# Optimization experiments

Hardware: AMD Instinct MI355X
Metric: run time of the kernel (lower is better)

## Reference

```python
import jax, jax.numpy as jnp
import numpy as np

B, N, F_IN, H, C, K = 32, 1024, 128, 64, 32, 2
L_HOP, NUM_ITER, TEMP = 2, 5, 0.5


def setup_inputs() -> dict:
    key = jax.random.key(0)
    ks = jax.random.split(key, 8)
    x = jax.random.normal(ks[0], (B, N, F_IN), jnp.float32)
    adj = jax.random.randint(ks[1], (B, N, N), 0, 2, jnp.int32)  # dense 0/1 adjacency per graph
    W_gcn = jax.random.normal(ks[2], (F_IN, H), jnp.float32) / np.sqrt(F_IN)
    b_gcn = jnp.zeros((H,), jnp.float32)
    W_unary = jax.random.normal(ks[3], (H, C), jnp.float32) / np.sqrt(H)
    b_unary = jnp.zeros((C,), jnp.float32)
    means = jax.random.normal(ks[4], (K, H), jnp.float32)
    scales = jnp.ones((K, H), jnp.float32) * 8.0  # widened so exp(-dist) stays in fp32 range
    kw = jnp.ones((K,), jnp.float32)
    mu = jax.random.normal(ks[5], (C, C), jnp.float32)
    return dict(x=x, adj=adj, W_gcn=W_gcn, b_gcn=b_gcn, W_unary=W_unary,
                b_unary=b_unary, means=means, scales=scales, kw=kw, mu=mu)


def _forward(x, adj_f, W_gcn, b_gcn, W_unary, b_unary, means, scales, kw, mu):
    n = x.shape[1]
    # --- GCN encode: D^{-1/2}(A+I)D^{-1/2} X W + b, relu ---
    a_hat = adj_f + jnp.eye(n, dtype=adj_f.dtype)
    dinv = jax.lax.rsqrt(a_hat.sum(-1))                       # [B,N], deg >= 1 via self-loop
    norm = dinv[:, :, None] * a_hat * dinv[:, None, :]        # [B,N,N]
    h = jax.nn.relu(jnp.einsum('bij,bjf,fh->bih', norm, x, W_gcn) + b_gcn)  # [B,N,H]
    # --- l-hop reachability mask ---
    adj_l = adj_f
    for _ in range(L_HOP - 1):
        adj_l = adj_l @ adj_f
    adj_l = (adj_l > 0).astype(h.dtype)                       # [B,N,N]
    # --- unary potentials ---
    unary = h @ W_unary + b_unary                             # [B,N,C]
    # --- Gaussian kernel: w_k * exp(dist_i[k] + dist_j[k]) == (e*w) @ e.T ---
    diff = (h[:, :, None, :] - means) / scales                # [B,N,K,H]
    e = jnp.exp(-jnp.sum(diff * diff, -1))                    # [B,N,K]
    pairwise = jnp.einsum('bik,k,bjk->bij', e, kw, e) * adj_l  # [B,N,N]
    # --- mean-field CRF iterations ---
    Q = jax.nn.softmax(unary, -1)
    for _ in range(NUM_ITER):
        msg = jnp.einsum('bij,bjc->bic', pairwise, Q @ mu)
        Q = jax.nn.softmax((unary + msg) / TEMP, -1)
    # --- soft-cluster pooling ---
    x_pooled = jnp.einsum('bnc,bnh->bch', Q, h)               # [B,C,H]
    adj_pooled = jnp.einsum('bnc,bnm,bmd->bcd', Q, adj_f, Q)  # [B,C,C]
    return x_pooled, adj_pooled


def reference(x, adj, W_gcn, b_gcn, W_unary, b_unary, means, scales, kw, mu):
    return _forward(x, adj.astype(x.dtype), W_gcn, b_gcn, W_unary, b_unary,
                    means, scales, kw, mu)
```

## Files before the change

### kernel.cpp

```cpp
#include <hip/hip_runtime.h>
#include <stdint.h>

#define NB  32
#define NN  1024
#define FIN 128
#define HH  64
#define CC  32
#define ZCAP 16
#define NITER 5

using short8  = __attribute__((ext_vector_type(8))) short;
using floatx4 = __attribute__((ext_vector_type(4))) float;

__device__ inline float b2f(unsigned short u) {
  union { uint32_t i; float f; } v; v.i = ((uint32_t)u) << 16; return v.f;
}
__device__ inline unsigned short f2b(float f) {
  union { uint32_t i; float f; } v; v.f = f;
  uint32_t r = v.i + 0x7FFFu + ((v.i >> 16) & 1u);
  return (unsigned short)(r >> 16);
}
__device__ inline floatx4 zf4() { floatx4 v = {0.f, 0.f, 0.f, 0.f}; return v; }

__global__ __launch_bounds__(256) void k_wcvt(const float* __restrict__ Wg,
    const float* __restrict__ Wu, unsigned short* __restrict__ Wgt,
    unsigned short* __restrict__ Wut, float* __restrict__ out, int out_n) {
  const int t = threadIdx.x;
  for (int idx = t; idx < HH * FIN; idx += 256) {
    int hh = idx >> 7, f = idx & 127;
    Wgt[idx] = f2b(Wg[f * HH + hh]);
  }
  for (int idx = t; idx < CC * HH; idx += 256) {
    int c = idx >> 6, f = idx & 63;
    Wut[idx] = f2b(Wu[f * CC + c]);
  }
  for (int idx = t; idx < out_n; idx += 256) out[idx] = 0.f;
}

__global__ __launch_bounds__(256) void k_bits(const int* __restrict__ adj,
    uint32_t* __restrict__ rowbits, float* __restrict__ dinv,
    int* __restrict__ zcnt) {
  __shared__ uint32_t rw[4][32];
  const int t = threadIdx.x, g = t >> 6, lane = t & 63;
  if (lane < 32) rw[g][lane] = 0u;
  __syncthreads();
  const size_t row = (size_t)blockIdx.x * 4 + g;
  int s = 0;
  #pragma unroll
  for (int rep = 0; rep < 4; rep++) {
    int4 a = ((const int4*)(adj + row * NN))[rep * 64 + lane];
    int b0 = (a.x != 0), b1 = (a.y != 0), b2 = (a.z != 0), b3 = (a.w != 0);
    uint32_t nib = ((uint32_t)(b0 | (b1 << 1) | (b2 << 2) | (b3 << 3))) << ((lane & 7) * 4);
    atomicOr(&rw[g][rep * 8 + (lane >> 3)], nib);
    s += b0 + b1 + b2 + b3;
  }
  #pragma unroll
  for (int m = 1; m < 64; m <<= 1) s += __shfl_xor(s, m, 64);
  __syncthreads();
  if (lane < 32) rowbits[row * 32 + lane] = rw[g][lane];
  if (lane == 0) { dinv[row] = rsqrtf((float)s + 1.0f); zcnt[row] = 0; }
}

__global__ __launch_bounds__(256) void k_cbits(const uint32_t* __restrict__ rowbits,
    uint32_t* __restrict__ colbits) {
  __shared__ uint32_t rbL[512 * 32];
  const int bid = blockIdx.x;
  const int b = bid >> 3, half = (bid >> 2) & 1, jt = bid & 3;
  const int t = threadIdx.x;
  const uint32_t* src = rowbits + ((size_t)b * NN + half * 512) * 32;
  for (int idx = t; idx < 512 * 32; idx += 256) rbL[idx] = src[idx];
  __syncthreads();
  const int j = jt * 256 + t, jw = j >> 5, jb = j & 31;
  uint32_t out[16];
  for (int w = 0; w < 16; w++) {
    uint32_t acc = 0;
    #pragma unroll
    for (int r = 0; r < 32; r++)
      acc |= ((rbL[(w * 32 + r) * 32 + jw] >> jb) & 1u) << r;
    out[w] = acc;
  }
  uint4* dst = (uint4*)(colbits + ((size_t)b * NN + j) * 32 + half * 16);
  #pragma unroll
  for (int x = 0; x < 4; x++) {
    uint4 v; v.x = out[4*x]; v.y = out[4*x+1]; v.z = out[4*x+2]; v.w = out[4*x+3];
    dst[x] = v;
  }
}

__global__ __launch_bounds__(256) void k_xw(const float* __restrict__ x,
    const unsigned short* __restrict__ Wgt, const float* __restrict__ dinv,
    unsigned short* __restrict__ xs, unsigned short* __restrict__ xst) {
  const int bid = blockIdx.x;
  const int b = bid >> 4;
  const int m0 = (bid & 15) * 64;
  const int t = threadIdx.x, wv = t >> 6, lane = t & 63, l15 = lane & 15, q = lane >> 4;
  const int mb = m0 + wv * 16;
  floatx4 acc[4];
  #pragma unroll
  for (int u = 0; u < 4; u++) acc[u] = zf4();
  #pragma unroll
  for (int k0 = 0; k0 < FIN; k0 += 32) {
    const float4* xp = (const float4*)(x + ((size_t)b * NN + mb + l15) * FIN + k0 + q * 8);
    float4 a0 = xp[0], a1 = xp[1];
    short8 af;
    af[0] = (short)f2b(a0.x); af[1] = (short)f2b(a0.y);
    af[2] = (short)f2b(a0.z); af[3] = (short)f2b(a0.w);
    af[4] = (short)f2b(a1.x); af[5] = (short)f2b(a1.y);
    af[6] = (short)f2b(a1.z); af[7] = (short)f2b(a1.w);
    #pragma unroll
    for (int u = 0; u < 4; u++) {
      short8 bf = *(const short8*)(Wgt + (u * 16 + l15) * FIN + k0 + q * 8);
      acc[u] = __builtin_amdgcn_mfma_f32_16x16x32_bf16(af, bf, acc[u], 0, 0, 0);
    }
  }
  #pragma unroll
  for (int r = 0; r < 4; r++) {
    const int i = mb + q * 4 + r;
    const float dv = dinv[b * NN + i];
    #pragma unroll
    for (int u = 0; u < 4; u++) {
      const int c = u * 16 + l15;
      unsigned short bv = f2b(dv * acc[u][r]);
      xs[((size_t)b * NN + i) * HH + c] = bv;
      xst[((size_t)b * HH + c) * NN + i] = bv;
    }
  }
}

__global__ __launch_bounds__(256) void k_gcnun(const uint32_t* __restrict__ rowbits,
    const unsigned short* __restrict__ xst, const unsigned short* __restrict__ xs,
    const float* __restrict__ dinv, const float* __restrict__ bg,
    const float* __restrict__ means, const float* __restrict__ scales,
    const unsigned short* __restrict__ Wut, const float* __restrict__ bu,
    float* __restrict__ h, float* __restrict__ e2, float* __restrict__ unary,
    float* __restrict__ Q0) {
  __shared__ unsigned short hsh[4][16][72];
  const int bid = blockIdx.x;
  const int b = bid >> 4;
  const int m0 = (bid & 15) * 64;
  const int t = threadIdx.x, wv = t >> 6, lane = t & 63, l15 = lane & 15, q = lane >> 4;
  const int mb = m0 + wv * 16;
  floatx4 acc[4];
  #pragma unroll
  for (int u = 0; u < 4; u++) acc[u] = zf4();
  const uint32_t* rbrow = rowbits + ((size_t)b * NN + mb + l15) * 32;
  for (int k0 = 0; k0 < NN; k0 += 32) {
    uint32_t sh = rbrow[k0 >> 5] >> (q * 8);
    short8 af;
    #pragma unroll
    for (int jj = 0; jj < 8; jj++)
      af[jj] = (short)(((sh >> jj) & 1u) ? 0x3F80 : 0);
    #pragma unroll
    for (int u = 0; u < 4; u++) {
      short8 bf = *(const short8*)(xst + ((size_t)b * HH + u * 16 + l15) * NN + k0 + q * 8);
      acc[u] = __builtin_amdgcn_mfma_f32_16x16x32_bf16(af, bf, acc[u], 0, 0, 0);
    }
  }
  float bgc[4], mn0[4], mn1[4], is0[4], is1[4];
  #pragma unroll
  for (int u = 0; u < 4; u++) {
    const int c = u * 16 + l15;
    bgc[u] = bg[c];
    mn0[u] = means[c];        is0[u] = 1.0f / scales[c];
    mn1[u] = means[HH + c];   is1[u] = 1.0f / scales[HH + c];
  }
  #pragma unroll
  for (int r = 0; r < 4; r++) {
    const int i = mb + q * 4 + r;
    const float dv = dinv[b * NN + i];
    float dd0 = 0.f, dd1 = 0.f;
    #pragma unroll
    for (int u = 0; u < 4; u++) {
      const int c = u * 16 + l15;
      float xsv = b2f(xs[((size_t)b * NN + i) * HH + c]);
      float v = dv * (acc[u][r] + xsv) + bgc[u];
      v = v > 0.f ? v : 0.f;
      h[((size_t)b * NN + i) * HH + c] = v;
      unsigned short hb = f2b(v);
      hsh[wv][q * 4 + r][c] = hb;
      float vb = b2f(hb);
      float t0 = (vb - mn0[u]) * is0[u]; dd0 += t0 * t0;
      float t1 = (vb - mn1[u]) * is1[u]; dd1 += t1 * t1;
    }
    #pragma unroll
    for (int m = 1; m < 16; m <<= 1) {
      dd0 += __shfl_xor(dd0, m, 64);
      dd1 += __shfl_xor(dd1, m, 64);
    }
    if (l15 == 0) {
      e2[((size_t)b * NN + i) * 2 + 0] = __expf(-dd0);
      e2[((size_t)b * NN + i) * 2 + 1] = __expf(-dd1);
    }
  }
  floatx4 uacc[2];
  uacc[0] = zf4(); uacc[1] = zf4();
  #pragma unroll
  for (int k0 = 0; k0 < HH; k0 += 32) {
    short8 af = *(const short8*)&hsh[wv][l15][k0 + q * 8];
    #pragma unroll
    for (int u = 0; u < 2; u++) {
      short8 bf = *(const short8*)(Wut + (u * 16 + l15) * HH + k0 + q * 8);
      uacc[u] = __builtin_amdgcn_mfma_f32_16x16x32_bf16(af, bf, uacc[u], 0, 0, 0);
    }
  }
  const float bu0 = bu[l15], bu1 = bu[16 + l15];
  #pragma unroll
  for (int r = 0; r < 4; r++) {
    const int i = mb + q * 4 + r;
    float a0 = uacc[0][r] + bu0;
    float a1 = uacc[1][r] + bu1;
    unary[((size_t)b * NN + i) * CC + l15] = a0;
    unary[((size_t)b * NN + i) * CC + 16 + l15] = a1;
    float mx = fmaxf(a0, a1);
    #pragma unroll
    for (int m = 1; m < 16; m <<= 1) mx = fmaxf(mx, __shfl_xor(mx, m, 64));
    float x0 = __expf(a0 - mx), x1 = __expf(a1 - mx);
    float s = x0 + x1;
    #pragma unroll
    for (int m = 1; m < 16; m <<= 1) s += __shfl_xor(s, m, 64);
    float inv = 1.f / s;
    Q0[((size_t)b * NN + i) * CC + l15] = x0 * inv;
    Q0[((size_t)b * NN + i) * CC + 16 + l15] = x1 * inv;
  }
}

__global__ __launch_bounds__(256) void k_zscan(const uint32_t* __restrict__ rowbits,
    const uint32_t* __restrict__ colbits, int* __restrict__ zcnt,
    int* __restrict__ zidx) {
  __shared__ uint32_t rwL[128 * 32];
  const int bid = blockIdx.x;
  const int b = bid >> 3, it = bid & 7;
  const int i0 = it * 128;
  const int t = threadIdx.x;
  #pragma unroll
  for (int x = 0; x < 16; x++)
    rwL[x * 256 + t] = rowbits[((size_t)b * NN + i0) * 32 + x * 256 + t];
  __syncthreads();
  for (int jc = 0; jc < 4; jc++) {
    const int j = jc * 256 + t;
    uint32_t cb[32];
    const uint4* cbp = (const uint4*)(colbits + ((size_t)b * NN + j) * 32);
    #pragma unroll
    for (int x = 0; x < 8; x++) {
      uint4 v = cbp[x];
      cb[4*x] = v.x; cb[4*x+1] = v.y; cb[4*x+2] = v.z; cb[4*x+3] = v.w;
    }
    for (int i = 0; i < 128; i++) {
      uint32_t m = 0;
      for (int w = 0; w < 32; w++) {
        m |= rwL[i * 32 + w] & cb[w];
        if (__all(m != 0)) break;
      }
      if (m == 0) {
        int old = atomicAdd(&zcnt[b * NN + i0 + i], 1);
        if (old < ZCAP) zidx[(size_t)(b * NN + i0 + i) * ZCAP + old] = j;
      }
    }
  }
}

__global__ __launch_bounds__(256) void k_titer(const float* __restrict__ e2,
    const float* __restrict__ Q, float* __restrict__ Tpart) {
  __shared__ float part[4][64];
  const int bid = blockIdx.x;
  const int b = bid >> 2, qd = bid & 3;
  const int t = threadIdx.x, kd = t & 63, d = t & 31, k = (t >> 5) & 1, sub = t >> 6;
  const float* e2b = e2 + (size_t)b * NN * 2;
  const float* Qb  = Q + (size_t)b * NN * CC;
  const int j0 = qd * 256 + sub * 64;
  float s = 0.f;
  #pragma unroll 8
  for (int jj = 0; jj < 64; jj++) {
    const int j = j0 + jj;
    s += e2b[j * 2 + k] * Qb[j * CC + d];
  }
  part[sub][kd] = s;
  __syncthreads();
  if (t < 64)
    Tpart[(size_t)bid * 64 + t] = part[0][t] + part[1][t] + part[2][t] + part[3][t];
}

__global__ __launch_bounds__(256) void k_supd(const float* __restrict__ unary,
    const float* __restrict__ e2, const float* __restrict__ Tpart,
    const float* __restrict__ mu, const float* __restrict__ kwp,
    const int* __restrict__ zcnt, const int* __restrict__ zidx,
    const uint32_t* __restrict__ rowbits, const uint32_t* __restrict__ colbits,
    const float* __restrict__ Qin, float* __restrict__ Qout,
    unsigned short* __restrict__ qtb, int last) {
  __shared__ float muL[CC * CC];
  __shared__ float Ts[64];
  __shared__ float S[64];
  const int bid = blockIdx.x;
  const int b = bid >> 2, seg = bid & 3;
  const int t = threadIdx.x;
  for (int i = t; i < CC * CC; i += 256) muL[i] = mu[i];
  if (t < 64)
    Ts[t] = Tpart[(size_t)(b * 4 + 0) * 64 + t] + Tpart[(size_t)(b * 4 + 1) * 64 + t]
          + Tpart[(size_t)(b * 4 + 2) * 64 + t] + Tpart[(size_t)(b * 4 + 3) * 64 + t];
  __syncthreads();
  if (t < 64) {
    const int k = t >> 5, c = t & 31;
    float s = 0.f;
    #pragma unroll 8
    for (int d = 0; d < CC; d++) s += Ts[k * 32 + d] * muL[d * 32 + c];
    S[t] = ((k == 0) ? kwp[0] : kwp[1]) * s;
  }
  __syncthreads();
  const int n = seg * 256 + t;
  const int gid = b * NN + n;
  const float e0 = e2[(size_t)gid * 2 + 0];
  const float e1 = e2[(size_t)gid * 2 + 1];
  float lg[CC];
  {
    const float4* urow = (const float4*)(unary + (size_t)gid * CC);
    const float4* S0 = (const float4*)S;
    const float4* S1 = (const float4*)(S + 32);
    #pragma unroll
    for (int c4 = 0; c4 < 8; c4++) {
      float4 uv = urow[c4], s0 = S0[c4], s1 = S1[c4];
      lg[c4*4]   = uv.x + e0 * s0.x + e1 * s1.x;
      lg[c4*4+1] = uv.y + e0 * s0.y + e1 * s1.y;
      lg[c4*4+2] = uv.z + e0 * s0.z + e1 * s1.z;
      lg[c4*4+3] = uv.w + e0 * s0.w + e1 * s1.w;
    }
  }
  const int zc = zcnt[gid];
  if (zc > 0) {
    const float kw0 = kwp[0], kw1 = kwp[1];
    if (zc <= ZCAP) {
      for (int z = 0; z < zc; z++) {
        const int j = zidx[(size_t)gid * ZCAP + z];
        const float w = kw0 * e0 * e2[((size_t)b * NN + j) * 2 + 0]
                      + kw1 * e1 * e2[((size_t)b * NN + j) * 2 + 1];
        const float* qj = Qin + ((size_t)b * NN + j) * CC;
        for (int d = 0; d < CC; d++) {
          const float wq = w * qj[d];
          #pragma unroll 8
          for (int c = 0; c < CC; c++) lg[c] -= wq * muL[d * CC + c];
        }
      }
    } else {
      const uint32_t* rbi = rowbits + (size_t)gid * 32;
      for (int j = 0; j < NN; j++) {
        uint32_t m = 0;
        const uint32_t* cbj = colbits + ((size_t)b * NN + j) * 32;
        for (int w32 = 0; w32 < 32; w32++) m |= rbi[w32] & cbj[w32];
        if (m == 0) {
          const float w = kw0 * e0 * e2[((size_t)b * NN + j) * 2 + 0]
                        + kw1 * e1 * e2[((size_t)b * NN + j) * 2 + 1];
          const float* qj = Qin + ((size_t)b * NN + j) * CC;
          for (int d = 0; d < CC; d++) {
            const float wq = w * qj[d];
            #pragma unroll 8
            for (int c = 0; c < CC; c++) lg[c] -= wq * muL[d * CC + c];
          }
        }
      }
    }
  }
  float mx = lg[0];
  #pragma unroll
  for (int c = 1; c < CC; c++) mx = fmaxf(mx, lg[c]);
  float s = 0.f;
  #pragma unroll
  for (int c = 0; c < CC; c++) { lg[c] = __expf((lg[c] - mx) * 2.0f); s += lg[c]; }
  float inv = 1.f / s;
  float4* qo = (float4*)(Qout + (size_t)gid * CC);
  #pragma unroll
  for (int c4 = 0; c4 < 8; c4++) {
    float4 v;
    v.x = lg[c4*4] * inv; v.y = lg[c4*4+1] * inv;
    v.z = lg[c4*4+2] * inv; v.w = lg[c4*4+3] * inv;
    qo[c4] = v;
  }
  if (last) {
    #pragma unroll
    for (int c = 0; c < CC; c++)
      qtb[((size_t)b * CC + c) * NN + n] = f2b(lg[c] * inv);
  }
}

__global__ __launch_bounds__(256) void k_adjq(const uint32_t* __restrict__ rowbits,
    const unsigned short* __restrict__ qtb, float* __restrict__ adjQ) {
  const int bid = blockIdx.x;
  const int b = bid >> 4;
  const int m0 = (bid & 15) * 64;
  const int t = threadIdx.x, wv = t >> 6, lane = t & 63, l15 = lane & 15, q = lane >> 4;
  const int mb = m0 + wv * 16;
  floatx4 acc[2];
  acc[0] = zf4(); acc[1] = zf4();
  const uint32_t* rbrow = rowbits + ((size_t)b * NN + mb + l15) * 32;
  for (int k0 = 0; k0 < NN; k0 += 32) {
    uint32_t sh = rbrow[k0 >> 5] >> (q * 8);
    short8 af;
    #pragma unroll
    for (int jj = 0; jj < 8; jj++)
      af[jj] = (short)(((sh >> jj) & 1u) ? 0x3F80 : 0);
    #pragma unroll
    for (int u = 0; u < 2; u++) {
      short8 bf = *(const short8*)(qtb + ((size_t)b * CC + u * 16 + l15) * NN + k0 + q * 8);
      acc[u] = __builtin_amdgcn_mfma_f32_16x16x32_bf16(af, bf, acc[u], 0, 0, 0);
    }
  }
  #pragma unroll
  for (int r = 0; r < 4; r++) {
    const int i = mb + q * 4 + r;
    #pragma unroll
    for (int u = 0; u < 2; u++)
      adjQ[((size_t)b * NN + i) * CC + u * 16 + l15] = acc[u][r];
  }
}

__global__ __launch_bounds__(256) void k_pool(const float* __restrict__ Q,
    const float* __restrict__ h, const float* __restrict__ adjQ,
    float* __restrict__ out) {
  const int bid = blockIdx.x;
  const int t = threadIdx.x;
  if (bid < NB * 4) {
    const int b = bid >> 2, jc = bid & 3;
    const int hh = t & 63, cg = t >> 6;
    float acc[8] = {0, 0, 0, 0, 0, 0, 0, 0};
    for (int jj = 0; jj < 256; jj++) {
      const int j = jc * 256 + jj;
      float hv = h[((size_t)b * NN + j) * HH + hh];
      const float* qr = Q + ((size_t)b * NN + j) * CC + cg * 8;
      #pragma unroll
      for (int k = 0; k < 8; k++) acc[k] += qr[k] * hv;
    }
    #pragma unroll
    for (int k = 0; k < 8; k++)
      atomicAdd(&out[((size_t)b * CC + cg * 8 + k) * HH + hh], acc[k]);
  } else {
    const int bid2 = bid - NB * 4;
    const int b = bid2 >> 2, jc = bid2 & 3;
    const int d = t & 31, cg = t >> 5;
    float acc[4] = {0, 0, 0, 0};
    for (int jj = 0; jj < 256; jj++) {
      const int j = jc * 256 + jj;
      float av = adjQ[((size_t)b * NN + j) * CC + d];
      const float* qr = Q + ((size_t)b * NN + j) * CC + cg * 4;
      #pragma unroll
      for (int k = 0; k < 4; k++) acc[k] += qr[k] * av;
    }
    #pragma unroll
    for (int k = 0; k < 4; k++)
      atomicAdd(&out[(size_t)NB * CC * HH + ((size_t)b * CC + cg * 4 + k) * CC + d], acc[k]);
  }
}

extern "C" void kernel_launch(void* const* d_in, const int* in_sizes, int n_in,
                              void* d_out, int out_size, void* d_ws, size_t ws_size,
                              hipStream_t stream) {
  (void)in_sizes; (void)n_in; (void)out_size;
  const float* x      = (const float*)d_in[0];
  const int*   adj    = (const int*)d_in[1];
  const float* Wg     = (const float*)d_in[2];
  const float* bg     = (const float*)d_in[3];
  const float* Wu     = (const float*)d_in[4];
  const float* bu     = (const float*)d_in[5];
  const float* means  = (const float*)d_in[6];
  const float* scales = (const float*)d_in[7];
  const float* kw     = (const float*)d_in[8];
  const float* mu     = (const float*)d_in[9];

  char* ws = (char*)d_ws;
  size_t off = 0;
  auto alloc = [&](size_t bytes) { char* p = ws + off; off += (bytes + 255) & ~(size_t)255; return p; };
  uint32_t*       rbits = (uint32_t*)alloc((size_t)NB * NN * 32 * 4);
  uint32_t*       cbits = (uint32_t*)alloc((size_t)NB * NN * 32 * 4);
  float*          dinv  = (float*)alloc((size_t)NB * NN * 4);
  unsigned short* Wgt   = (unsigned short*)alloc((size_t)HH * FIN * 2);
  unsigned short* Wut   = (unsigned short*)alloc((size_t)CC * HH * 2);
  unsigned short* xs    = (unsigned short*)alloc((size_t)NB * NN * HH * 2);
  unsigned short* xst   = (unsigned short*)alloc((size_t)NB * HH * NN * 2);
  float*          h     = (float*)alloc((size_t)NB * NN * HH * 4);
  float*          e2    = (float*)alloc((size_t)NB * NN * 2 * 4);
  float*          unary = (float*)alloc((size_t)NB * NN * CC * 4);
  int*            zcnt  = (int*)alloc((size_t)NB * NN * 4);
  int*            zidx  = (int*)alloc((size_t)NB * NN * ZCAP * 4);
  float*          Qa    = (float*)alloc((size_t)NB * NN * CC * 4);
  float*          Qb    = (float*)alloc((size_t)NB * NN * CC * 4);
  unsigned short* qtb   = (unsigned short*)alloc((size_t)NB * CC * NN * 2);
  float*          adjQ  = (float*)alloc((size_t)NB * NN * CC * 4);
  float*          Tpart = (float*)alloc((size_t)NB * 4 * 64 * 4);
  if (off > ws_size) return;

  float* out = (float*)d_out;
  const int out_n = NB * CC * (HH + CC);

  k_wcvt <<<1, 256, 0, stream>>>(Wg, Wu, Wgt, Wut, out, out_n);
  k_bits <<<NB * NN / 4, 256, 0, stream>>>(adj, rbits, dinv, zcnt);
  k_cbits<<<NB * 8, 256, 0, stream>>>(rbits, cbits);
  k_xw   <<<NB * 16, 256, 0, stream>>>(x, Wgt, dinv, xs, xst);
  k_gcnun<<<NB * 16, 256, 0, stream>>>(rbits, xst, xs, dinv, bg, means, scales,
                                       Wut, bu, h, e2, unary, Qa);
  k_zscan<<<NB * 8, 256, 0, stream>>>(rbits, cbits, zcnt, zidx);
  float* qin = Qa; float* qout = Qb;
  for (int it = 0; it < NITER; it++) {
    k_titer<<<NB * 4, 256, 0, stream>>>(e2, qin, Tpart);
    k_supd <<<NB * 4, 256, 0, stream>>>(unary, e2, Tpart, mu, kw, zcnt, zidx,
                                        rbits, cbits, qin, qout, qtb,
                                        it == NITER - 1 ? 1 : 0);
    float* tmp = qin; qin = qout; qout = tmp;
  }
  k_adjq <<<NB * 16, 256, 0, stream>>>(rbits, qtb, adjQ);
  k_pool <<<NB * 8, 256, 0, stream>>>(qin, h, adjQ, out);
}
```

Before: 428.9 us.

## Fuse all CRF iterations and pooling into a single per-graph LDS-resident kernel

Replaces the ten per-iteration titer/supd launches with one kernel that keeps each graph's Q (packed bf16) and e2 in shared memory and runs all five mean-field iterations with block-level syncs. The initial softmax moves into this kernel, and Q·h pooling is fused at its end. The adjacency-Q product and the adj pooling are merged into one kernel through shared-memory staging. This removes launch overhead and global Q round trips, but each graph's redundant 4 blocks each recompute all 1024 nodes, and Q is held in bf16 during iterations, lowering precision.

```diff
diff --git a/kernel.cpp b/kernel.cpp
--- a/kernel.cpp
+++ b/kernel.cpp
@@ -14,6 +14,12 @@
 
 __device__ inline float b2f(unsigned short u) {
   union { uint32_t i; float f; } v; v.i = ((uint32_t)u) << 16; return v.f;
+}
+__device__ inline float b2f_lo(uint32_t w) {
+  union { uint32_t i; float f; } v; v.i = w << 16; return v.f;
+}
+__device__ inline float b2f_hi(uint32_t w) {
+  union { uint32_t i; float f; } v; v.i = w & 0xFFFF0000u; return v.f;
 }
 __device__ inline unsigned short f2b(float f) {
   union { uint32_t i; float f; } v; v.f = f;
@@ -132,8 +138,7 @@
     const float* __restrict__ dinv, const float* __restrict__ bg,
     const float* __restrict__ means, const float* __restrict__ scales,
     const unsigned short* __restrict__ Wut, const float* __restrict__ bu,
-    float* __restrict__ h, float* __restrict__ e2, float* __restrict__ unary,
-    float* __restrict__ Q0) {
+    float* __restrict__ h, float* __restrict__ e2, float* __restrict__ unary) {
   __shared__ unsigned short hsh[4][16][72];
   const int bid = blockIdx.x;
   const int b = bid >> 4;
@@ -207,20 +212,8 @@
   #pragma unroll
   for (int r = 0; r < 4; r++) {
     const int i = mb + q * 4 + r;
-    float a0 = uacc[0][r] + bu0;
-    float a1 = uacc[1][r] + bu1;
-    unary[((size_t)b * NN + i) * CC + l15] = a0;
-    unary[((size_t)b * NN + i) * CC + 16 + l15] = a1;
-    float mx = fmaxf(a0, a1);
-    #pragma unroll
-    for (int m = 1; m < 16; m <<= 1) mx = fmaxf(mx, __shfl_xor(mx, m, 64));
-    float x0 = __expf(a0 - mx), x1 = __expf(a1 - mx);
-    float s = x0 + x1;
-    #pragma unroll
-    for (int m = 1; m < 16; m <<= 1) s += __shfl_xor(s, m, 64);
-    float inv = 1.f / s;
-    Q0[((size_t)b * NN + i) * CC + l15] = x0 * inv;
-    Q0[((size_t)b * NN + i) * CC + 16 + l15] = x1 * inv;
+    unary[((size_t)b * NN + i) * CC + l15] = uacc[0][r] + bu0;
+    unary[((size_t)b * NN + i) * CC + 16 + l15] = uacc[1][r] + bu1;
   }
 }
 
@@ -259,129 +252,173 @@
   }
 }
 
-__global__ __launch_bounds__(256) void k_titer(const float* __restrict__ e2,
-    const float* __restrict__ Q, float* __restrict__ Tpart) {
+__global__ __launch_bounds__(256) void k_crf1(const float* __restrict__ unary,
+    const float* __restrict__ e2g, const float* __restrict__ kwp,
+    const float* __restrict__ mu, const uint32_t* __restrict__ rowbits,
+    const uint32_t* __restrict__ colbits, const int* __restrict__ zcnt,
+    const int* __restrict__ zidx, const float* __restrict__ h,
+    unsigned short* __restrict__ qtb, float* __restrict__ out) {
+  __shared__ uint32_t QLu[NN * 17];
+  __shared__ float eL[NN * 2];
+  __shared__ float muL[CC * CC];
   __shared__ float part[4][64];
-  const int bid = blockIdx.x;
-  const int b = bid >> 2, qd = bid & 3;
-  const int t = threadIdx.x, kd = t & 63, d = t & 31, k = (t >> 5) & 1, sub = t >> 6;
-  const float* e2b = e2 + (size_t)b * NN * 2;
-  const float* Qb  = Q + (size_t)b * NN * CC;
-  const int j0 = qd * 256 + sub * 64;
-  float s = 0.f;
-  #pragma unroll 8
-  for (int jj = 0; jj < 64; jj++) {
-    const int j = j0 + jj;
-    s += e2b[j * 2 + k] * Qb[j * CC + d];
-  }
-  part[sub][kd] = s;
-  __syncthreads();
-  if (t < 64)
-    Tpart[(size_t)bid * 64 + t] = part[0][t] + part[1][t] + part[2][t] + part[3][t];
-}
-
-__global__ __launch_bounds__(256) void k_supd(const float* __restrict__ unary,
-    const float* __restrict__ e2, const float* __restrict__ Tpart,
-    const float* __restrict__ mu, const float* __restrict__ kwp,
-    const int* __restrict__ zcnt, const int* __restrict__ zidx,
-    const uint32_t* __restrict__ rowbits, const uint32_t* __restrict__ colbits,
-    const float* __restrict__ Qin, float* __restrict__ Qout,
-    unsigned short* __restrict__ qtb, int last) {
-  __shared__ float muL[CC * CC];
-  __shared__ float Ts[64];
+  __shared__ float Tf[64];
   __shared__ float S[64];
   const int bid = blockIdx.x;
   const int b = bid >> 2, seg = bid & 3;
   const int t = threadIdx.x;
+  const float kw0 = kwp[0], kw1 = kwp[1];
   for (int i = t; i < CC * CC; i += 256) muL[i] = mu[i];
-  if (t < 64)
-    Ts[t] = Tpart[(size_t)(b * 4 + 0) * 64 + t] + Tpart[(size_t)(b * 4 + 1) * 64 + t]
-          + Tpart[(size_t)(b * 4 + 2) * 64 + t] + Tpart[(size_t)(b * 4 + 3) * 64 + t];
+  for (int n = t; n < NN; n += 256) {
+    float2 ev = ((const float2*)(e2g + ((size_t)b * NN + n) * 2))[0];
+    eL[n * 2] = ev.x; eL[n * 2 + 1] = ev.y;
+    float lg[CC];
+    const float4* ur = (const float4*)(unary + ((size_t)b * NN + n) * CC);
+    #pragma unroll
+    for (int c4 = 0; c4 < 8; c4++) {
+      float4 v = ur[c4];
+      lg[c4*4] = v.x; lg[c4*4+1] = v.y; lg[c4*4+2] = v.z; lg[c4*4+3] = v.w;
+    }
+    float mx = lg[0];
+    #pragma unroll
+    for (int c = 1; c < CC; c++) mx = fmaxf(mx, lg[c]);
+    float s = 0.f;
+    #pragma unroll
+    for (int c = 0; c < CC; c++) { lg[c] = __expf(lg[c] - mx); s += lg[c]; }
+    float inv = 1.f / s;
+    #pragma unroll
+    for (int d2 = 0; d2 < 16; d2++)
+      QLu[n * 17 + d2] = (uint32_t)f2b(lg[2*d2] * inv)
+                       | ((uint32_t)f2b(lg[2*d2+1] * inv) << 16);
+  }
   __syncthreads();
-  if (t < 64) {
-    const int k = t >> 5, c = t & 31;
+  const int kd = t & 63, dd = t & 31, kk = (t >> 5) & 1, sub = t >> 6;
+  for (int it = 0; it < NITER; it++) {
     float s = 0.f;
-    #pragma unroll 8
-    for (int d = 0; d < CC; d++) s += Ts[k * 32 + d] * muL[d * 32 + c];
-    S[t] = ((k == 0) ? kwp[0] : kwp[1]) * s;
-  }
-  __syncthreads();
-  const int n = seg * 256 + t;
-  const int gid = b * NN + n;
-  const float e0 = e2[(size_t)gid * 2 + 0];
-  const float e1 = e2[(size_t)gid * 2 + 1];
-  float lg[CC];
-  {
-    const float4* urow = (const float4*)(unary + (size_t)gid * CC);
-    const float4* S0 = (const float4*)S;
-    const float4* S1 = (const float4*)(S + 32);
-    #pragma unroll
-    for (int c4 = 0; c4 < 8; c4++) {
-      float4 uv = urow[c4], s0 = S0[c4], s1 = S1[c4];
-      lg[c4*4]   = uv.x + e0 * s0.x + e1 * s1.x;
-      lg[c4*4+1] = uv.y + e0 * s0.y + e1 * s1.y;
-      lg[c4*4+2] = uv.z + e0 * s0.z + e1 * s1.z;
-      lg[c4*4+3] = uv.w + e0 * s0.w + e1 * s1.w;
-    }
-  }
-  const int zc = zcnt[gid];
-  if (zc > 0) {
-    const float kw0 = kwp[0], kw1 = kwp[1];
-    if (zc <= ZCAP) {
-      for (int z = 0; z < zc; z++) {
-        const int j = zidx[(size_t)gid * ZCAP + z];
-        const float w = kw0 * e0 * e2[((size_t)b * NN + j) * 2 + 0]
-                      + kw1 * e1 * e2[((size_t)b * NN + j) * 2 + 1];
-        const float* qj = Qin + ((size_t)b * NN + j) * CC;
-        for (int d = 0; d < CC; d++) {
-          const float wq = w * qj[d];
-          #pragma unroll 8
-          for (int c = 0; c < CC; c++) lg[c] -= wq * muL[d * CC + c];
+    for (int jj = 0; jj < 256; jj++) {
+      const int j = sub * 256 + jj;
+      const float ej = eL[j * 2 + kk];
+      const uint32_t w = QLu[j * 17 + (dd >> 1)];
+      s += ej * ((dd & 1) ? b2f_hi(w) : b2f_lo(w));
+    }
+    part[sub][kd] = s;
+    __syncthreads();
+    if (t < 64) Tf[t] = part[0][t] + part[1][t] + part[2][t] + part[3][t];
+    __syncthreads();
+    if (t < 64) {
+      const int k = t >> 5, c = t & 31;
+      float ss = 0.f;
+      #pragma unroll 8
+      for (int d = 0; d < CC; d++) ss += Tf[k * 32 + d] * muL[d * 32 + c];
+      S[t] = ((k == 0) ? kw0 : kw1) * ss;
+    }
+    __syncthreads();
+    uint32_t newq[4][16];
+    #pragma unroll
+    for (int rep = 0; rep < 4; rep++) {
+      const int n = rep * 256 + t;
+      const float e0 = eL[n * 2], e1 = eL[n * 2 + 1];
+      float lg[CC];
+      {
+        const float4* ur = (const float4*)(unary + ((size_t)b * NN + n) * CC);
+        const float4* S0 = (const float4*)S;
+        const float4* S1 = (const float4*)(S + 32);
+        #pragma unroll
+        for (int c4 = 0; c4 < 8; c4++) {
+          float4 uv = ur[c4], s0 = S0[c4], s1 = S1[c4];
+          lg[c4*4]   = uv.x + e0 * s0.x + e1 * s1.x;
+          lg[c4*4+1] = uv.y + e0 * s0.y + e1 * s1.y;
+          lg[c4*4+2] = uv.z + e0 * s0.z + e1 * s1.z;
+          lg[c4*4+3] = uv.w + e0 * s0.w + e1 * s1.w;
         }
       }
-    } else {
-      const uint32_t* rbi = rowbits + (size_t)gid * 32;
-      for (int j = 0; j < NN; j++) {
-        uint32_t m = 0;
-        const uint32_t* cbj = colbits + ((size_t)b * NN + j) * 32;
-        for (int w32 = 0; w32 < 32; w32++) m |= rbi[w32] & cbj[w32];
-        if (m == 0) {
-          const float w = kw0 * e0 * e2[((size_t)b * NN + j) * 2 + 0]
-                        + kw1 * e1 * e2[((size_t)b * NN + j) * 2 + 1];
-          const float* qj = Qin + ((size_t)b * NN + j) * CC;
-          for (int d = 0; d < CC; d++) {
-            const float wq = w * qj[d];
-            #pragma unroll 8
-            for (int c = 0; c < CC; c++) lg[c] -= wq * muL[d * CC + c];
+      const int zc = zcnt[b * NN + n];
+      if (zc > 0) {
+        if (zc <= ZCAP) {
+          for (int z = 0; z < zc; z++) {
+            const int j = zidx[(size_t)(b * NN + n) * ZCAP + z];
+            const float w = kw0 * e0 * eL[j * 2] + kw1 * e1 * eL[j * 2 + 1];
+            for (int d2 = 0; d2 < 16; d2++) {
+              const uint32_t wq = QLu[j * 17 + d2];
+              const float w0 = w * b2f_lo(wq), w1 = w * b2f_hi(wq);
+              #pragma unroll 8
+              for (int c = 0; c < CC; c++)
+                lg[c] -= w0 * muL[(2*d2) * 32 + c] + w1 * muL[(2*d2+1) * 32 + c];
+            }
+          }
+        } else {
+          const uint32_t* rbi = rowbits + ((size_t)b * NN + n) * 32;
+          for (int j = 0; j < NN; j++) {
+            uint32_t m = 0;
+            const uint32_t* cbj = colbits + ((size_t)b * NN + j) * 32;
+            for (int w32 = 0; w32 < 32; w32++) m |= rbi[w32] & cbj[w32];
+            if (m == 0) {
+              const float w = kw0 * e0 * eL[j * 2] + kw1 * e1 * eL[j * 2 + 1];
+              for (int d2 = 0; d2 < 16; d2++) {
+                const uint32_t wq = QLu[j * 17 + d2];
+                const float w0 = w * b2f_lo(wq), w1 = w * b2f_hi(wq);
+                #pragma unroll 8
+                for (int c = 0; c < CC; c++)
+                  lg[c] -= w0 * muL[(2*d2) * 32 + c] + w1 * muL[(2*d2+1) * 32 + c];
+              }
+            }
           }
         }
       }
-    }
-  }
-  float mx = lg[0];
-  #pragma unroll
-  for (int c = 1; c < CC; c++) mx = fmaxf(mx, lg[c]);
-  float s = 0.f;
-  #pragma unroll
-  for (int c = 0; c < CC; c++) { lg[c] = __expf((lg[c] - mx) * 2.0f); s += lg[c]; }
-  float inv = 1.f / s;
-  float4* qo = (float4*)(Qout + (size_t)gid * CC);
-  #pragma unroll
-  for (int c4 = 0; c4 < 8; c4++) {
-    float4 v;
-    v.x = lg[c4*4] * inv; v.y = lg[c4*4+1] * inv;
-    v.z = lg[c4*4+2] * inv; v.w = lg[c4*4+3] * inv;
-    qo[c4] = v;
-  }
-  if (last) {
-    #pragma unroll
-    for (int c = 0; c < CC; c++)
-      qtb[((size_t)b * CC + c) * NN + n] = f2b(lg[c] * inv);
-  }
-}
-
-__global__ __launch_bounds__(256) void k_adjq(const uint32_t* __restrict__ rowbits,
-    const unsigned short* __restrict__ qtb, float* __restrict__ adjQ) {
+      float mx = lg[0];
+      #pragma unroll
+      for (int c = 1; c < CC; c++) mx = fmaxf(mx, lg[c]);
+      float ss = 0.f;
+      #pragma unroll
+      for (int c = 0; c < CC; c++) { lg[c] = __expf((lg[c] - mx) * 2.0f); ss += lg[c]; }
+      const float inv = 1.f / ss;
+      #pragma unroll
+      for (int d2 = 0; d2 < 16; d2++)
+        newq[rep][d2] = (uint32_t)f2b(lg[2*d2] * inv)
+                      | ((uint32_t)f2b(lg[2*d2+1] * inv) << 16);
+    }
+    __syncthreads();
+    #pragma unroll
+    for (int rep = 0; rep < 4; rep++) {
+      const int n = rep * 256 + t;
+      #pragma unroll
+      for (int d2 = 0; d2 < 16; d2++) QLu[n * 17 + d2] = newq[rep][d2];
+    }
+    __syncthreads();
+  }
+  {
+    const int n = seg * 256 + t;
+    #pragma unroll
+    for (int d2 = 0; d2 < 16; d2++) {
+      const uint32_t w = QLu[n * 17 + d2];
+      qtb[((size_t)b * CC + 2*d2) * NN + n]     = (unsigned short)(w & 0xFFFFu);
+      qtb[((size_t)b * CC + 2*d2 + 1) * NN + n] = (unsigned short)(w >> 16);
+    }
+  }
+  {
+    const int hh = t & 63, cg = t >> 6;
+    float acc[8] = {0, 0, 0, 0, 0, 0, 0, 0};
+    const int j0 = seg * 256;
+    for (int jj = 0; jj < 256; jj++) {
+      const int j = j0 + jj;
+      const float hv = h[((size_t)b * NN + j) * HH + hh];
+      #pragma unroll
+      for (int w = 0; w < 4; w++) {
+        const uint32_t q2 = QLu[j * 17 + cg * 4 + w];
+        acc[2*w]     += b2f_lo(q2) * hv;
+        acc[2*w + 1] += b2f_hi(q2) * hv;
+      }
+    }
+    #pragma unroll
+    for (int k = 0; k < 8; k++)
+      atomicAdd(&out[((size_t)b * CC + cg * 8 + k) * HH + hh], acc[k]);
+  }
+}
+
+__global__ __launch_bounds__(256) void k_adjqp(const uint32_t* __restrict__ rowbits,
+    const unsigned short* __restrict__ qtb, float* __restrict__ out) {
+  __shared__ float adjL[64][33];
+  __shared__ float qL[64][32];
   const int bid = blockIdx.x;
   const int b = bid >> 4;
   const int m0 = (bid & 15) * 64;
@@ -403,49 +440,27 @@
     }
   }
   #pragma unroll
-  for (int r = 0; r < 4; r++) {
-    const int i = mb + q * 4 + r;
+  for (int r = 0; r < 4; r++)
     #pragma unroll
     for (int u = 0; u < 2; u++)
-      adjQ[((size_t)b * NN + i) * CC + u * 16 + l15] = acc[u][r];
-  }
-}
-
-__global__ __launch_bounds__(256) void k_pool(const float* __restrict__ Q,
-    const float* __restrict__ h, const float* __restrict__ adjQ,
-    float* __restrict__ out) {
-  const int bid = blockIdx.x;
-  const int t = threadIdx.x;
-  if (bid < NB * 4) {
-    const int b = bid >> 2, jc = bid & 3;
-    const int hh = t & 63, cg = t >> 6;
-    float acc[8] = {0, 0, 0, 0, 0, 0, 0, 0};
-    for (int jj = 0; jj < 256; jj++) {
-      const int j = jc * 256 + jj;
-      float hv = h[((size_t)b * NN + j) * HH + hh];
-      const float* qr = Q + ((size_t)b * NN + j) * CC + cg * 8;
-      #pragma unroll
-      for (int k = 0; k < 8; k++) acc[k] += qr[k] * hv;
-    }
-    #pragma unroll
-    for (int k = 0; k < 8; k++)
-      atomicAdd(&out[((size_t)b * CC + cg * 8 + k) * HH + hh], acc[k]);
-  } else {
-    const int bid2 = bid - NB * 4;
-    const int b = bid2 >> 2, jc = bid2 & 3;
-    const int d = t & 31, cg = t >> 5;
-    float acc[4] = {0, 0, 0, 0};
-    for (int jj = 0; jj < 256; jj++) {
-      const int j = jc * 256 + jj;
-      float av = adjQ[((size_t)b * NN + j) * CC + d];
-      const float* qr = Q + ((size_t)b * NN + j) * CC + cg * 4;
-      #pragma unroll
-      for (int k = 0; k < 4; k++) acc[k] += qr[k] * av;
-    }
-    #pragma unroll
-    for (int k = 0; k < 4; k++)
-      atomicAdd(&out[(size_t)NB * CC * HH + ((size_t)b * CC + cg * 4 + k) * CC + d], acc[k]);
-  }
+      adjL[wv * 16 + q * 4 + r][u * 16 + l15] = acc[u][r];
+  #pragma unroll
+  for (int x = 0; x < 8; x++) {
+    const int idx = x * 256 + t;
+    const int i = idx & 63, c = idx >> 6;
+    qL[i][c] = b2f(qtb[((size_t)b * CC + c) * NN + m0 + i]);
+  }
+  __syncthreads();
+  const int d = t & 31, cg = t >> 5;
+  float a2[4] = {0, 0, 0, 0};
+  for (int i = 0; i < 64; i++) {
+    const float av = adjL[i][d];
+    #pragma unroll
+    for (int k = 0; k < 4; k++) a2[k] += qL[i][cg * 4 + k] * av;
+  }
+  #pragma unroll
+  for (int k = 0; k < 4; k++)
+    atomicAdd(&out[(size_t)NB * CC * HH + ((size_t)b * CC + cg * 4 + k) * CC + d], a2[k]);
 }
 
 extern "C" void kernel_launch(void* const* d_in, const int* in_sizes, int n_in,
@@ -478,11 +493,7 @@
   float*          unary = (float*)alloc((size_t)NB * NN * CC * 4);
   int*            zcnt  = (int*)alloc((size_t)NB * NN * 4);
   int*            zidx  = (int*)alloc((size_t)NB * NN * ZCAP * 4);
-  float*          Qa    = (float*)alloc((size_t)NB * NN * CC * 4);
-  float*          Qb    = (float*)alloc((size_t)NB * NN * CC * 4);
   unsigned short* qtb   = (unsigned short*)alloc((size_t)NB * CC * NN * 2);
-  float*          adjQ  = (float*)alloc((size_t)NB * NN * CC * 4);
-  float*          Tpart = (float*)alloc((size_t)NB * 4 * 64 * 4);
   if (off > ws_size) return;
 
   float* out = (float*)d_out;
@@ -491,18 +502,11 @@
   k_wcvt <<<1, 256, 0, stream>>>(Wg, Wu, Wgt, Wut, out, out_n);
   k_bits <<<NB * NN / 4, 256, 0, stream>>>(adj, rbits, dinv, zcnt);
   k_cbits<<<NB * 8, 256, 0, stream>>>(rbits, cbits);
+  k_zscan<<<NB * 8, 256, 0, stream>>>(rbits, cbits, zcnt, zidx);
   k_xw   <<<NB * 16, 256, 0, stream>>>(x, Wgt, dinv, xs, xst);
   k_gcnun<<<NB * 16, 256, 0, stream>>>(rbits, xst, xs, dinv, bg, means, scales,
-                                       Wut, bu, h, e2, unary, Qa);
-  k_zscan<<<NB * 8, 256, 0, stream>>>(rbits, cbits, zcnt, zidx);
-  float* qin = Qa; float* qout = Qb;
-  for (int it = 0; it < NITER; it++) {
-    k_titer<<<NB * 4, 256, 0, stream>>>(e2, qin, Tpart);
-    k_supd <<<NB * 4, 256, 0, stream>>>(unary, e2, Tpart, mu, kw, zcnt, zidx,
-                                        rbits, cbits, qin, qout, qtb,
-                                        it == NITER - 1 ? 1 : 0);
-    float* tmp = qin; qin = qout; qout = tmp;
-  }
-  k_adjq <<<NB * 16, 256, 0, stream>>>(rbits, qtb, adjQ);
-  k_pool <<<NB * 8, 256, 0, stream>>>(qin, h, adjQ, out);
-}
+                                       Wut, bu, h, e2, unary);
+  k_crf1 <<<NB * 4, 256, 0, stream>>>(unary, e2, kw, mu, rbits, cbits,
+                                      zcnt, zidx, h, qtb, out);
+  k_adjqp<<<NB * 16, 256, 0, stream>>>(rbits, qtb, out);
+}
```

Measured after the change: 437.8 us. +2.1%, slower.
